# Performance work log

Hardware: AMD Instinct MI355X
Metric: run time of the kernel (lower is better)

## Reference

```python
import jax, jax.numpy as jnp
import numpy as np

EMB = 1024
FF = 4 * EMB

def _ternary(w):
    # BitNet b1.58 absmean quantization; forward uses pure ternary weights
    scale = jnp.maximum(jnp.mean(jnp.abs(w)), 1e-8)
    w_t = jnp.clip(jnp.round(w / scale), -1.0, 1.0)
    # STE: forward = w_t, backward = identity w.r.t. w
    return w + jax.lax.stop_gradient(w_t - w)

def setup_inputs() -> dict:
    key = jax.random.key(0)
    kx, k1, k2, kb1, kb2 = jax.random.split(key, 5)
    x = jax.random.normal(kx, (4, 2048, EMB), dtype=jnp.float32)
    # nn.Linear default init: U(-1/sqrt(fan_in), 1/sqrt(fan_in))
    lim1 = 1.0 / np.sqrt(EMB)
    lim2 = 1.0 / np.sqrt(FF)
    W1 = jax.random.uniform(k1, (FF, EMB), jnp.float32, -lim1, lim1)
    b1 = jax.random.uniform(kb1, (FF,), jnp.float32, -lim1, lim1)
    W2 = jax.random.uniform(k2, (EMB, FF), jnp.float32, -lim2, lim2)
    b2 = jax.random.uniform(kb2, (EMB,), jnp.float32, -lim2, lim2)
    return {"x": x, "W1": W1, "b1": b1, "W2": W2, "b2": b2}

def reference(x, W1, b1, W2, b2):
    h = jnp.einsum('bsd,fd->bsf', x, _ternary(W1)) + b1  # [B,S,FF]
    h = jax.nn.gelu(h, approximate=False)  # torch nn.GELU default = exact erf
    out = jnp.einsum('bsf,df->bsd', h, _ternary(W2)) + b2  # [B,S,EMB]
    return out
```

## Files before the change

kernel.cpp:

```cpp
#include <hip/hip_runtime.h>
#include <hip/hip_bf16.h>
#include <cstdint>
#include <cstddef>

typedef __bf16 bf16x8 __attribute__((ext_vector_type(8)));
typedef float  f32x4  __attribute__((ext_vector_type(4)));

__device__ __forceinline__ unsigned short f2bf(float f) {
    __hip_bfloat16 b = __float2bfloat16(f);
    return *reinterpret_cast<unsigned short*>(&b);
}

__device__ __forceinline__ float fast_gelu(float x) {
    float x2 = x * x;
    float m  = x * __builtin_fmaf(x2, -0.10294314f, -2.30220795f);
    float e  = __builtin_amdgcn_exp2f(m);
    return x * __builtin_amdgcn_rcpf(1.0f + e);
}


__global__ void abs_sum_cvt_kernel(const float4* __restrict__ w0, const float4* __restrict__ w1,
                                   int n4w, float* __restrict__ part,
                                   const float4* __restrict__ x, ushort4* __restrict__ xb,
                                   int n4x) {
    int seg = (int)blockIdx.x >> 9;
    int b = (int)blockIdx.x & 511;
    if (seg == 2) {
        for (int i = b * blockDim.x + threadIdx.x; i < n4x; i += 512 * blockDim.x) {
            float4 v = x[i];
            ushort4 o;
            o.x = f2bf(v.x); o.y = f2bf(v.y); o.z = f2bf(v.z); o.w = f2bf(v.w);
            xb[i] = o;
        }
        return;
    }
    const float4* w = seg ? w1 : w0;
    float s = 0.0f;
    for (int i = b * blockDim.x + threadIdx.x; i < n4w; i += 512 * blockDim.x) {
        float4 v = w[i];
        s += fabsf(v.x) + fabsf(v.y) + fabsf(v.z) + fabsf(v.w);
    }
    #pragma unroll
    for (int o = 32; o > 0; o >>= 1) s += __shfl_down(s, o, 64);
    __shared__ float ps[4];
    int lane = threadIdx.x & 63, wid = threadIdx.x >> 6;
    if (lane == 0) ps[wid] = s;
    __syncthreads();
    if (threadIdx.x == 0) part[blockIdx.x] = ps[0] + ps[1] + ps[2] + ps[3];
}

__global__ void ternarize_kernel(const float4* __restrict__ w0, ushort4* __restrict__ t0,
                                 const float4* __restrict__ w1, ushort4* __restrict__ t1,
                                 int n4w, const float* __restrict__ part, float inv_n) {
    int seg = (int)blockIdx.x >> 10;
    int b = (int)blockIdx.x & 1023;

    float s = 0.0f;
    for (int j = threadIdx.x; j < 512; j += 256) s += part[seg * 512 + j];
    #pragma unroll
    for (int o = 32; o > 0; o >>= 1) s += __shfl_down(s, o, 64);
    __shared__ float ps[4];
    __shared__ float sscale;
    int lane = threadIdx.x & 63, wid = threadIdx.x >> 6;
    if (lane == 0) ps[wid] = s;
    __syncthreads();
    if (threadIdx.x == 0) {
        float tot = ps[0] + ps[1] + ps[2] + ps[3];
        sscale = fmaxf(tot * inv_n, 1e-8f);
    }
    __syncthreads();
    float inv = 1.0f / sscale;

    const float4* w = seg ? w1 : w0;
    ushort4* t = seg ? t1 : t0;
    for (int i = b * blockDim.x + threadIdx.x; i < n4w; i += 1024 * blockDim.x) {
        float4 v = w[i];
        ushort4 o;
        o.x = f2bf(fminf(fmaxf(rintf(v.x * inv), -1.0f), 1.0f));
        o.y = f2bf(fminf(fmaxf(rintf(v.y * inv), -1.0f), 1.0f));
        o.z = f2bf(fminf(fmaxf(rintf(v.z * inv), -1.0f), 1.0f));
        o.w = f2bf(fminf(fmaxf(rintf(v.w * inv), -1.0f), 1.0f));
        t[i] = o;
    }
}


template <int EPI, int K, int N>
__global__ __launch_bounds__(256)
void gemm_bt_kernel(const unsigned short* __restrict__ A,
                    const unsigned short* __restrict__ B,
                    const float* __restrict__ bias,
                    void* __restrict__ C) {
    __shared__ __align__(16) unsigned short As[128 * 64];
    __shared__ __align__(16) unsigned short Bs[128 * 64];

    const int tid  = threadIdx.x;
    const int lane = tid & 63;
    const int wid  = tid >> 6;
    const int mBase = (wid >> 1) * 64;
    const int nBase = (wid & 1) * 64;
    const int lr = lane & 15;
    const int lq = lane >> 4;

    const size_t aRow0 = (size_t)blockIdx.y * 128;
    const size_t bRow0 = (size_t)blockIdx.x * 128;

    const int rA  = tid >> 3;
    const int cSw = (((tid & 7) ^ (rA & 7)) << 3);
    const unsigned short* ga = A + (aRow0 + rA) * (size_t)K + cSw;
    const unsigned short* gb = B + (bRow0 + rA) * (size_t)K + cSw;
    unsigned short* ldsA = &As[tid * 8];
    unsigned short* ldsB = &Bs[tid * 8];

    f32x4 acc[4][4];
    #pragma unroll
    for (int i = 0; i < 4; ++i)
        #pragma unroll
        for (int j = 0; j < 4; ++j)
            acc[i][j] = f32x4{0.f, 0.f, 0.f, 0.f};

    const int swz0 = ((lq ^ (lr & 7)) << 3);
    const int swz1 = (((4 + lq) ^ (lr & 7)) << 3);

    #pragma unroll 2
    for (int k0 = 0; k0 < K; k0 += 64) {
        __syncthreads();
        #pragma unroll
        for (int t = 0; t < 4; ++t) {
            __builtin_amdgcn_global_load_lds(
                (const __attribute__((address_space(1))) void*)(ga + (size_t)t * 32 * K),
                (__attribute__((address_space(3))) void*)(ldsA + t * 2048), 16, 0, 0);
            __builtin_amdgcn_global_load_lds(
                (const __attribute__((address_space(1))) void*)(gb + (size_t)t * 32 * K),
                (__attribute__((address_space(3))) void*)(ldsB + t * 2048), 16, 0, 0);
        }
        ga += 64;
        gb += 64;
        __syncthreads();
        #pragma unroll
        for (int ks = 0; ks < 2; ++ks) {
            const int swz = ks ? swz1 : swz0;
            bf16x8 avec[4], bvec[4];
            #pragma unroll
            for (int i = 0; i < 4; ++i) {
                avec[i] = *(const bf16x8*)&As[(mBase + i * 16 + lr) * 64 + swz];
                bvec[i] = *(const bf16x8*)&Bs[(nBase + i * 16 + lr) * 64 + swz];
            }
            #pragma unroll
            for (int mi = 0; mi < 4; ++mi)
                #pragma unroll
                for (int ni = 0; ni < 4; ++ni)
                    acc[mi][ni] = __builtin_amdgcn_mfma_f32_16x16x32_bf16(
                        avec[mi], bvec[ni], acc[mi][ni], 0, 0, 0);
        }
    }

    #pragma unroll
    for (int mi = 0; mi < 4; ++mi) {
        #pragma unroll
        for (int ni = 0; ni < 4; ++ni) {
            int col = (int)bRow0 + nBase + ni * 16 + lr;
            float bv = bias[col];
            #pragma unroll
            for (int r = 0; r < 4; ++r) {
                size_t row = aRow0 + mBase + mi * 16 + lq * 4 + r;
                float v = acc[mi][ni][r] + bv;
                if (EPI == 0) {
                    ((unsigned short*)C)[row * (size_t)N + col] = f2bf(fast_gelu(v));
                } else {
                    ((float*)C)[row * (size_t)N + col] = v;
                }
            }
        }
    }
}


extern "C" void kernel_launch(void* const* d_in, const int* in_sizes, int n_in,
                              void* d_out, int out_size, void* d_ws, size_t ws_size,
                              hipStream_t stream) {
    const float* x  = (const float*)d_in[0];
    const float* W1 = (const float*)d_in[1];
    const float* b1 = (const float*)d_in[2];
    const float* W2 = (const float*)d_in[3];
    const float* b2 = (const float*)d_in[4];
    float* out = (float*)d_out;

    const int M = 8192, EMB = 1024, FF = 4096;
    const int nW = FF * EMB;

    char* ws = (char*)d_ws;
    float* part = (float*)ws;
    unsigned short* W1t = (unsigned short*)(ws + 16384);
    unsigned short* W2t = W1t + (size_t)nW;
    unsigned short* xb  = W2t + (size_t)nW;
    unsigned short* h   = xb  + (size_t)M * EMB;

    abs_sum_cvt_kernel<<<1536, 256, 0, stream>>>((const float4*)W1, (const float4*)W2,
                                                 nW / 4, part,
                                                 (const float4*)x, (ushort4*)xb,
                                                 (M * EMB) / 4);
    ternarize_kernel<<<2048, 256, 0, stream>>>((const float4*)W1, (ushort4*)W1t,
                                               (const float4*)W2, (ushort4*)W2t,
                                               nW / 4, part, 1.0f / nW);

    gemm_bt_kernel<0, 1024, 4096><<<dim3(FF / 128, M / 128), 256, 0, stream>>>(xb, W1t, b1, h);
    gemm_bt_kernel<1, 4096, 1024><<<dim3(EMB / 128, M / 128), 256, 0, stream>>>(h, W2t, b2, out);
}
```

Baseline: 267.4 us.

## Rewrite GEMMs as 8-wave double-buffered pipelined kernels with larger tiles

Replaces the 128x128, 4-wave GEMM with a 256xBN tile, 8-wave kernel. It double-buffers LDS and interleaves global->LDS staging with MFMA phases using explicit barriers, waitcnts and setprio. It also swizzles block ids for L2 locality. The aim is to hide load latency and raise data reuse per tile, at the cost of more LDS and registers, which may limit occupancy, and a fragile hand-written schedule.

New measurement: 268.6 us. No clear change (+0.4%).

```diff
diff --git a/kernel.cpp b/kernel.cpp
--- a/kernel.cpp
+++ b/kernel.cpp
@@ -85,87 +85,201 @@
 }
 
 
-template <int EPI, int K, int N>
-__global__ __launch_bounds__(256)
-void gemm_bt_kernel(const unsigned short* __restrict__ A,
-                    const unsigned short* __restrict__ B,
-                    const float* __restrict__ bias,
-                    void* __restrict__ C) {
-    __shared__ __align__(16) unsigned short As[128 * 64];
-    __shared__ __align__(16) unsigned short Bs[128 * 64];
+#define GLL(SRC, DST) __builtin_amdgcn_global_load_lds( \
+    (const __attribute__((address_space(1))) void*)(SRC), \
+    (__attribute__((address_space(3))) void*)(DST), 16, 0, 0)
+
+#define BAR() do { asm volatile("" ::: "memory"); \
+    __builtin_amdgcn_sched_barrier(0); \
+    __builtin_amdgcn_s_barrier(); \
+    __builtin_amdgcn_sched_barrier(0); \
+    asm volatile("" ::: "memory"); } while (0)
+
+#define WAIT_LGKM() do { asm volatile("s_waitcnt lgkmcnt(0)" ::: "memory"); \
+    __builtin_amdgcn_sched_barrier(0); } while (0)
+
+#define WAIT_VM4() do { asm volatile("s_waitcnt vmcnt(4)" ::: "memory"); \
+    __builtin_amdgcn_sched_barrier(0); } while (0)
+
+#define LDA(MS, BUF) do { \
+    _Pragma("unroll") \
+    for (int f_ = 0; f_ < MF2; ++f_) { \
+        const unsigned short* p_ = &As[(BUF)*16384 + AH*8192 + (rA0 + (MS)*(WM/2) + f_*16 + lr)*64]; \
+        av[MS][f_][0] = *(const bf16x8*)(p_ + swz0); \
+        av[MS][f_][1] = *(const bf16x8*)(p_ + swz1); \
+    } \
+} while (0)
+
+#define LDB(NS, BUF) do { \
+    _Pragma("unroll") \
+    for (int g_ = 0; g_ < NF2; ++g_) { \
+        const unsigned short* p_ = &Bs[(BUF)*(BN*64) + BHw*(BH*64) + (rB0 + (NS)*32 + g_*16 + lr)*64]; \
+        bv[NS][g_][0] = *(const bf16x8*)(p_ + swz0); \
+        bv[NS][g_][1] = *(const bf16x8*)(p_ + swz1); \
+    } \
+} while (0)
+
+#define MMA(MS, NS) do { \
+    __builtin_amdgcn_s_setprio(1); \
+    _Pragma("unroll") \
+    for (int f_ = 0; f_ < MF2; ++f_) { \
+        _Pragma("unroll") \
+        for (int g_ = 0; g_ < NF2; ++g_) { \
+            acc[(MS)*MF2 + f_][(NS)*NF2 + g_] = __builtin_amdgcn_mfma_f32_16x16x32_bf16( \
+                av[MS][f_][0], bv[NS][g_][0], acc[(MS)*MF2 + f_][(NS)*NF2 + g_], 0, 0, 0); \
+            acc[(MS)*MF2 + f_][(NS)*NF2 + g_] = __builtin_amdgcn_mfma_f32_16x16x32_bf16( \
+                av[MS][f_][1], bv[NS][g_][1], acc[(MS)*MF2 + f_][(NS)*NF2 + g_], 0, 0, 0); \
+        } \
+    } \
+    __builtin_amdgcn_s_setprio(0); \
+} while (0)
+
+#define STAGE_A(BUF, H, T) do { \
+    const unsigned short* s_ = pA + (size_t)((H)*128)*K + (((T) & (KT-1)) << 6); \
+    GLL(s_,                 &As[(BUF)*16384 + (H)*8192 + tid*8]); \
+    GLL(s_ + (size_t)64*K,  &As[(BUF)*16384 + (H)*8192 + 4096 + tid*8]); \
+} while (0)
+
+#define STAGE_B(BUF, H, T) do { \
+    const unsigned short* s_ = pB + (size_t)((H)*BH)*K + (((T) & (KT-1)) << 6); \
+    GLL(s_, &Bs[(BUF)*(BN*64) + (H)*(BH*64) + tid*8]); \
+    if constexpr (BN == 256) { \
+        GLL(s_ + (size_t)64*K, &Bs[(BUF)*(BN*64) + (H)*(BH*64) + 4096 + tid*8]); \
+    } \
+} while (0)
+
+template <int EPI, int K, int N, int BN, int WM>
+__global__ __launch_bounds__(512, 2)
+void gemm8p_kernel(const unsigned short* __restrict__ A,
+                   const unsigned short* __restrict__ B,
+                   const float* __restrict__ bias,
+                   void* __restrict__ C) {
+    constexpr int BM = 256;
+    constexpr int WN = 64;
+    constexpr int WARPS_N = BN / WN;
+    constexpr int MF = WM / 16;
+    constexpr int NF = WN / 16;
+    constexpr int MF2 = MF / 2;
+    constexpr int NF2 = NF / 2;
+    constexpr int BH = (BN == 256) ? 128 : 64;
+    constexpr int KT = K / 64;
+    constexpr int NBX = N / BN;
+    static_assert((BM / WM) * WARPS_N == 8, "8 waves");
+    static_assert((KT & (KT - 1)) == 0, "KT pow2");
+
+    __shared__ __align__(16) unsigned short As[2 * 256 * 64];
+    __shared__ __align__(16) unsigned short Bs[2 * BN * 64];
 
     const int tid  = threadIdx.x;
     const int lane = tid & 63;
     const int wid  = tid >> 6;
-    const int mBase = (wid >> 1) * 64;
-    const int nBase = (wid & 1) * 64;
     const int lr = lane & 15;
     const int lq = lane >> 4;
-
-    const size_t aRow0 = (size_t)blockIdx.y * 128;
-    const size_t bRow0 = (size_t)blockIdx.x * 128;
-
-    const int rA  = tid >> 3;
-    const int cSw = (((tid & 7) ^ (rA & 7)) << 3);
-    const unsigned short* ga = A + (aRow0 + rA) * (size_t)K + cSw;
-    const unsigned short* gb = B + (bRow0 + rA) * (size_t)K + cSw;
-    unsigned short* ldsA = &As[tid * 8];
-    unsigned short* ldsB = &Bs[tid * 8];
-
-    f32x4 acc[4][4];
-    #pragma unroll
-    for (int i = 0; i < 4; ++i)
-        #pragma unroll
-        for (int j = 0; j < 4; ++j)
-            acc[i][j] = f32x4{0.f, 0.f, 0.f, 0.f};
+    const int mb = wid / WARPS_N;
+    const int nb = wid % WARPS_N;
+
+    const int nwg = (int)gridDim.x;
+    const int bid = (int)blockIdx.x;
+    const int swz = (bid & 7) * (nwg >> 3) + (bid >> 3);
+    const int bx = swz % NBX;
+    const int by = swz / NBX;
+    const size_t aRow0 = (size_t)by * BM;
+    const size_t bRow0 = (size_t)bx * BN;
+
+    const int sRow = tid >> 3;
+    const int sChunk = ((tid & 7) ^ (sRow & 7)) << 3;
+    const unsigned short* pA = A + (aRow0 + sRow) * (size_t)K + sChunk;
+    const unsigned short* pB = B + (bRow0 + sRow) * (size_t)K + sChunk;
 
     const int swz0 = ((lq ^ (lr & 7)) << 3);
     const int swz1 = (((4 + lq) ^ (lr & 7)) << 3);
-
-    #pragma unroll 2
-    for (int k0 = 0; k0 < K; k0 += 64) {
-        __syncthreads();
+    const int AH  = (mb * WM) >> 7;
+    const int rA0 = (mb * WM) & 127;
+    const int BHw = (nb * WN) / BH;
+    const int rB0 = (nb * WN) % BH;
+
+    f32x4 acc[MF][NF];
+    #pragma unroll
+    for (int i_ = 0; i_ < MF; ++i_)
         #pragma unroll
-        for (int t = 0; t < 4; ++t) {
-            __builtin_amdgcn_global_load_lds(
-                (const __attribute__((address_space(1))) void*)(ga + (size_t)t * 32 * K),
-                (__attribute__((address_space(3))) void*)(ldsA + t * 2048), 16, 0, 0);
-            __builtin_amdgcn_global_load_lds(
-                (const __attribute__((address_space(1))) void*)(gb + (size_t)t * 32 * K),
-                (__attribute__((address_space(3))) void*)(ldsB + t * 2048), 16, 0, 0);
-        }
-        ga += 64;
-        gb += 64;
-        __syncthreads();
+        for (int j_ = 0; j_ < NF; ++j_)
+            acc[i_][j_] = f32x4{0.f, 0.f, 0.f, 0.f};
+
+    bf16x8 av[2][MF2][2];
+    bf16x8 bv[2][NF2][2];
+
+    STAGE_B(0, 0, 0); STAGE_B(0, 1, 0);
+    STAGE_A(0, 0, 0); STAGE_A(0, 1, 0);
+    STAGE_A(1, 0, 1); STAGE_A(1, 1, 1);
+    WAIT_VM4();
+    BAR();
+
+    #pragma unroll 1
+    for (int it = 0; it < K / 128; ++it) {
+        const int tO  = 2 * it + 1;
+        const int tN0 = 2 * it + 2;
+        const int tN1 = 2 * it + 3;
+
+        LDA(0, 0); LDB(0, 0);
+        STAGE_B(1, 0, tO);
+        BAR(); WAIT_LGKM();
+        MMA(0, 0);
+        BAR();
+
+        LDA(1, 0);
+        STAGE_B(1, 1, tO);
+        BAR(); WAIT_LGKM();
+        MMA(1, 0);
+        BAR();
+
+        LDB(1, 0);
+        STAGE_A(0, 0, tN0);
+        BAR(); WAIT_LGKM();
+        MMA(1, 1);
+        BAR();
+
+        STAGE_A(0, 1, tN0);
+        WAIT_VM4();
+        BAR();
+        MMA(0, 1);
+        BAR();
+
+        LDA(0, 1); LDB(0, 1);
+        STAGE_B(0, 0, tN0);
+        BAR(); WAIT_LGKM();
+        MMA(0, 0);
+        BAR();
+
+        LDA(1, 1);
+        STAGE_B(0, 1, tN0);
+        BAR(); WAIT_LGKM();
+        MMA(1, 0);
+        BAR();
+
+        LDB(1, 1);
+        STAGE_A(1, 0, tN1);
+        BAR(); WAIT_LGKM();
+        MMA(1, 1);
+        BAR();
+
+        STAGE_A(1, 1, tN1);
+        WAIT_VM4();
+        BAR();
+        MMA(0, 1);
+        BAR();
+    }
+
+    #pragma unroll
+    for (int mf = 0; mf < MF; ++mf) {
         #pragma unroll
-        for (int ks = 0; ks < 2; ++ks) {
-            const int swz = ks ? swz1 : swz0;
-            bf16x8 avec[4], bvec[4];
-            #pragma unroll
-            for (int i = 0; i < 4; ++i) {
-                avec[i] = *(const bf16x8*)&As[(mBase + i * 16 + lr) * 64 + swz];
-                bvec[i] = *(const bf16x8*)&Bs[(nBase + i * 16 + lr) * 64 + swz];
-            }
-            #pragma unroll
-            for (int mi = 0; mi < 4; ++mi)
-                #pragma unroll
-                for (int ni = 0; ni < 4; ++ni)
-                    acc[mi][ni] = __builtin_amdgcn_mfma_f32_16x16x32_bf16(
-                        avec[mi], bvec[ni], acc[mi][ni], 0, 0, 0);
-        }
-    }
-
-    #pragma unroll
-    for (int mi = 0; mi < 4; ++mi) {
-        #pragma unroll
-        for (int ni = 0; ni < 4; ++ni) {
-            int col = (int)bRow0 + nBase + ni * 16 + lr;
-            float bv = bias[col];
+        for (int nf = 0; nf < NF; ++nf) {
+            const size_t col = bRow0 + (size_t)nb * WN + nf * 16 + lr;
+            const float bvs = bias[col];
             #pragma unroll
             for (int r = 0; r < 4; ++r) {
-                size_t row = aRow0 + mBase + mi * 16 + lq * 4 + r;
-                float v = acc[mi][ni][r] + bv;
-                if (EPI == 0) {
+                const size_t row = aRow0 + (size_t)mb * WM + mf * 16 + lq * 4 + r;
+                float v = acc[mf][nf][r] + bvs;
+                if constexpr (EPI == 0) {
                     ((unsigned short*)C)[row * (size_t)N + col] = f2bf(fast_gelu(v));
                 } else {
                     ((float*)C)[row * (size_t)N + col] = v;
@@ -174,6 +288,16 @@
         }
     }
 }
+
+#undef GLL
+#undef BAR
+#undef WAIT_LGKM
+#undef WAIT_VM4
+#undef LDA
+#undef LDB
+#undef MMA
+#undef STAGE_A
+#undef STAGE_B
 
 
 extern "C" void kernel_launch(void* const* d_in, const int* in_sizes, int n_in,
@@ -204,6 +328,6 @@
                                                (const float4*)W2, (ushort4*)W2t,
                                                nW / 4, part, 1.0f / nW);
 
-    gemm_bt_kernel<0, 1024, 4096><<<dim3(FF / 128, M / 128), 256, 0, stream>>>(xb, W1t, b1, h);
-    gemm_bt_kernel<1, 4096, 1024><<<dim3(EMB / 128, M / 128), 256, 0, stream>>>(h, W2t, b2, out);
-}
+    gemm8p_kernel<0, 1024, 4096, 256, 128><<<dim3(512), dim3(512), 0, stream>>>(xb, W1t, b1, h);
+    gemm8p_kernel<1, 4096, 1024, 128, 64><<<dim3(256), dim3(512), 0, stream>>>(h, W2t, b2, out);
+}
```
